# Performance work log

Hardware: AMD Instinct MI355X
Metric: run time of the kernel (lower is better)

Reference implementation:

```python
import jax, jax.numpy as jnp
import numpy as np
import math

B, L, D, H = 2, 2048, 1024, 16
HD = D // H

def setup_inputs() -> dict:
    key = jax.random.key(0)
    ks = jax.random.split(key, 8)
    s = 1.0 / math.sqrt(D)
    # causal additive mask: 0 on/below diagonal, -inf above
    causal = jnp.where(jnp.tril(jnp.ones((L, L), dtype=bool)), 0.0, -jnp.inf)
    causal = causal[None, None].astype(jnp.float32)  # [1,1,L,L]
    return {
        "Q": jax.random.normal(ks[0], (B, L, D), jnp.float32),
        "K": jax.random.normal(ks[1], (B, L, D), jnp.float32),
        "V": jax.random.normal(ks[2], (B, L, D), jnp.float32),
        "attn_mask": causal,
        "padding_mask": jnp.zeros((B, L), dtype=bool),
        "wq": jax.random.normal(ks[3], (D, D), jnp.float32) * s,
        "wk": jax.random.normal(ks[4], (D, D), jnp.float32) * s,
        "wv": jax.random.normal(ks[5], (D, D), jnp.float32) * s,
        "wout": jax.random.normal(ks[6], (D, D), jnp.float32) * s,
    }

def reference(Q, K, V, attn_mask, padding_mask, wq, wk, wv, wout):
    b, l, _ = Q.shape
    # projections (torch Linear: x @ W.T); weights sampled as [out,in]-like square
    def proj(x, w):
        return (x @ w.T).reshape(b, l, H, HD).transpose(0, 2, 1, 3)  # [B,H,L,hd]
    q = proj(Q, wq)
    k = proj(K, wk)
    v = proj(V, wv)
    scores = jnp.einsum("bhqd,bhkd->bhqk", q, k) / math.sqrt(HD)
    scores = scores + attn_mask
    scores = jnp.where(padding_mask[:, None, None, :], -jnp.inf, scores)
    weights = jax.nn.softmax(scores, axis=-1)
    ctx = jnp.einsum("bhqk,bhkd->bhqd", weights, v)
    ctx = ctx.transpose(0, 2, 1, 3).reshape(b, l, D)
    return ctx @ wout.T
```

## Files before the change

kernel.cpp:

```cpp
#include <hip/hip_runtime.h>
#include <stdint.h>
#include <stddef.h>

typedef __bf16 bf16_t;
typedef bf16_t bf16x4 __attribute__((ext_vector_type(4)));
typedef bf16_t bf16x8 __attribute__((ext_vector_type(8)));
typedef float f32x4 __attribute__((ext_vector_type(4)));

#define MFMA_BF16(A_, B_, C_) __builtin_amdgcn_mfma_f32_16x16x32_bf16(A_, B_, C_, 0, 0, 0)

static constexpr int Lseq = 2048;
static constexpr int Dmod = 1024;
static constexpr int Hn   = 16;
static constexpr int HDim = 64;
static constexpr size_t M1 = 1u << 20;

__device__ __forceinline__ int swz(int row, int chunk) {
  return row * 64 + ((chunk ^ (row & 7)) << 3);
}

__device__ __forceinline__ void async_ld16(const bf16_t* g, bf16_t* l) {
  __builtin_amdgcn_global_load_lds(
      (const __attribute__((address_space(1))) void*)g,
      (__attribute__((address_space(3))) void*)l, 16, 0, 0);
}

__global__ __launch_bounds__(256) void cvt_kernel(
    const float* __restrict__ Q, const float* __restrict__ K,
    const float* __restrict__ V, const float* __restrict__ wq,
    const float* __restrict__ wk, const float* __restrict__ wv,
    const float* __restrict__ wout, bf16_t* __restrict__ wsb)
{
  const int s = blockIdx.z;
  const float* __restrict__ src;
  if      (s < 4)   src = Q    + (size_t)s * M1;
  else if (s < 8)   src = K    + (size_t)(s - 4) * M1;
  else if (s < 12)  src = V    + (size_t)(s - 8) * M1;
  else if (s == 12) src = wq;
  else if (s == 13) src = wk;
  else if (s == 14) src = wv;
  else              src = wout;
  bf16_t* __restrict__ dst = wsb + (size_t)s * M1;

  const int t = blockIdx.x * 256 + threadIdx.x;
#pragma unroll
  for (int j = 0; j < 4; ++j) {
    const int i4 = t + j * 65536;
    float4 v4 = ((const float4*)src)[i4];
    bf16x4 b4;
    b4[0] = (bf16_t)v4.x; b4[1] = (bf16_t)v4.y;
    b4[2] = (bf16_t)v4.z; b4[3] = (bf16_t)v4.w;
    ((bf16x4*)dst)[i4] = b4;
  }
}

__global__ __launch_bounds__(256) void proj_kernel(
    const bf16_t* __restrict__ Qbf, const bf16_t* __restrict__ Kbf,
    const bf16_t* __restrict__ Vbf, const bf16_t* __restrict__ wqb,
    const bf16_t* __restrict__ wkb, const bf16_t* __restrict__ wvb,
    bf16_t* __restrict__ qo, bf16_t* __restrict__ ko, bf16_t* __restrict__ vo)
{
  const int z = blockIdx.z;
  const bf16_t* __restrict__ A  = (z == 0) ? Qbf : (z == 1) ? Kbf : Vbf;
  const bf16_t* __restrict__ Bw = (z == 0) ? wqb : (z == 1) ? wkb : wvb;
  bf16_t* __restrict__ dst      = (z == 0) ? qo  : (z == 1) ? ko  : vo;

  __shared__ __align__(16) bf16_t As[128 * 64];
  __shared__ __align__(16) bf16_t Bs[128 * 64];

  const int tid  = threadIdx.x;
  const int wave = tid >> 6;
  const int lane = tid & 63;
  const int quad = lane >> 4;
  const int l16  = lane & 15;
  const int wm   = (wave & 1) * 64;
  const int wn   = (wave >> 1) * 64;
  const int m0   = blockIdx.y * 128;
  const int n0   = blockIdx.x * 128;

  const int srow8  = lane >> 3;
  const int schunk = (lane & 7) ^ srow8;

  f32x4 acc[4][4];
#pragma unroll
  for (int i = 0; i < 4; ++i)
#pragma unroll
    for (int j = 0; j < 4; ++j)
#pragma unroll
      for (int e = 0; e < 4; ++e) acc[i][j][e] = 0.0f;

  for (int kt = 0; kt < 16; ++kt) {
    const int k0 = kt * 64;
    __syncthreads();
#pragma unroll
    for (int i = 0; i < 4; ++i) {
      const int rb = wave * 32 + i * 8;
      async_ld16(&A [(size_t)(m0 + rb + srow8) * Dmod + k0 + schunk * 8], &As[rb * 64]);
      async_ld16(&Bw[(size_t)(n0 + rb + srow8) * Dmod + k0 + schunk * 8], &Bs[rb * 64]);
    }
    __syncthreads();

    bf16x8 af[4][2], bfr[4][2];
#pragma unroll
    for (int mt = 0; mt < 4; ++mt) {
      const int row = wm + mt * 16 + l16;
      af[mt][0] = *(const bf16x8*)&As[swz(row, quad)];
      af[mt][1] = *(const bf16x8*)&As[swz(row, quad + 4)];
    }
#pragma unroll
    for (int nt = 0; nt < 4; ++nt) {
      const int row = wn + nt * 16 + l16;
      bfr[nt][0] = *(const bf16x8*)&Bs[swz(row, quad)];
      bfr[nt][1] = *(const bf16x8*)&Bs[swz(row, quad + 4)];
    }
#pragma unroll
    for (int mt = 0; mt < 4; ++mt)
#pragma unroll
      for (int nt = 0; nt < 4; ++nt) {
        acc[mt][nt] = MFMA_BF16(af[mt][0], bfr[nt][0], acc[mt][nt]);
        acc[mt][nt] = MFMA_BF16(af[mt][1], bfr[nt][1], acc[mt][nt]);
      }
  }

#pragma unroll
  for (int mt = 0; mt < 4; ++mt) {
    const int grb = m0 + wm + mt * 16 + quad * 4;
    const int bb  = grb >> 11;
    const int lb  = grb & 2047;
#pragma unroll
    for (int nt = 0; nt < 4; ++nt) {
      const int gc = n0 + wn + nt * 16 + l16;
      const int h  = gc >> 6;
      const int hd = gc & 63;
      if (z == 2) {
        bf16x4 pk;
#pragma unroll
        for (int r = 0; r < 4; ++r) pk[r] = (bf16_t)acc[mt][nt][r];
        *(bf16x4*)&dst[(((size_t)(bb * Hn + h) * HDim + hd) << 11) + lb] = pk;
      } else {
#pragma unroll
        for (int r = 0; r < 4; ++r)
          dst[(((size_t)(bb * Hn + h) * Lseq + lb + r) << 6) + hd] = (bf16_t)acc[mt][nt][r];
      }
    }
  }
}

__global__ __launch_bounds__(256) void attn_kernel(
    const bf16_t* __restrict__ q, const bf16_t* __restrict__ k,
    const bf16_t* __restrict__ v, bf16_t* __restrict__ ctx)
{
  const int px = blockIdx.x;
  const int bh = blockIdx.y;
  const int bb = bh >> 4;
  const int h  = bh & 15;

  const int tid  = threadIdx.x;
  const int wave = tid >> 6;
  const int lane = tid & 63;
  const int quad = lane >> 4;
  const int l16  = lane & 15;

  __shared__ __align__(16) bf16_t Ks[2][64 * 64];
  __shared__ __align__(16) bf16_t Vs[2][64 * 64];
  __shared__ __align__(16) bf16_t Ps[4][16][72];

  const bf16_t* __restrict__ qb = q + (size_t)bh * (Lseq * HDim);
  const bf16_t* __restrict__ kb = k + (size_t)bh * (Lseq * HDim);
  const bf16_t* __restrict__ vb = v + (size_t)bh * (HDim * Lseq);

  const int srow8  = lane >> 3;
  const int schunk = (lane & 7) ^ srow8;

  bf16x8 ones;
#pragma unroll
  for (int i = 0; i < 8; ++i) ones[i] = (bf16_t)1.0f;

  for (int half = 0; half < 2; ++half) {
    const int qt = half ? (31 - px) : px;
    const int q0 = qt * 64;
    const int qrow = q0 + wave * 16 + l16;

    bf16x8 qf0 = *(const bf16x8*)&qb[(size_t)qrow * HDim + quad * 8];
    bf16x8 qf1 = *(const bf16x8*)&qb[(size_t)qrow * HDim + 32 + quad * 8];

    f32x4 o[4];
    f32x4 lacc;
#pragma unroll
    for (int e = 0; e < 4; ++e) lacc[e] = 0.0f;
#pragma unroll
    for (int nt = 0; nt < 4; ++nt)
#pragma unroll
      for (int e = 0; e < 4; ++e) o[nt][e] = 0.0f;

    __syncthreads();
#pragma unroll
    for (int i = 0; i < 2; ++i) {
      const int rb = wave * 16 + i * 8;
      const int r  = rb + srow8;
      async_ld16(&kb[(size_t)r * HDim + schunk * 8], &Ks[0][rb * 64]);
      async_ld16(&vb[(size_t)r * Lseq + schunk * 8], &Vs[0][rb * 64]);
    }

    for (int jt = 0; jt <= qt; ++jt) {
      const int cur = jt & 1;
      __syncthreads();

      if (jt < qt) {
        const int j1 = (jt + 1) * 64;
#pragma unroll
        for (int i = 0; i < 2; ++i) {
          const int rb = wave * 16 + i * 8;
          const int r  = rb + srow8;
          async_ld16(&kb[(size_t)(j1 + r) * HDim + schunk * 8], &Ks[cur ^ 1][rb * 64]);
          async_ld16(&vb[(size_t)r * Lseq + j1 + schunk * 8], &Vs[cur ^ 1][rb * 64]);
        }
      }

      f32x4 s[4];
#pragma unroll
      for (int nt = 0; nt < 4; ++nt) {
#pragma unroll
        for (int e = 0; e < 4; ++e) s[nt][e] = 0.0f;
        const int krow = nt * 16 + l16;
        bf16x8 kf0 = *(const bf16x8*)&Ks[cur][swz(krow, quad)];
        bf16x8 kf1 = *(const bf16x8*)&Ks[cur][swz(krow, quad + 4)];
        s[nt] = MFMA_BF16(kf0, qf0, s[nt]);
        s[nt] = MFMA_BF16(kf1, qf1, s[nt]);
      }

      const bool diag = (jt == qt);
#pragma unroll
      for (int nt = 0; nt < 4; ++nt) {
        bf16x4 pk;
#pragma unroll
        for (int r = 0; r < 4; ++r) {
          float val = s[nt][r] * 0.18033688f;
          if (diag && (nt * 16 + quad * 4 + r > wave * 16 + l16)) val = -1e30f;
          pk[r] = (bf16_t)__builtin_amdgcn_exp2f(val);
        }
        *(bf16x4*)&Ps[wave][l16][nt * 16 + quad * 4] = pk;
      }

      bf16x8 pf0 = *(const bf16x8*)&Ps[wave][l16][quad * 8];
      bf16x8 pf1 = *(const bf16x8*)&Ps[wave][l16][32 + quad * 8];

      lacc = MFMA_BF16(pf0, ones, lacc);
      lacc = MFMA_BF16(pf1, ones, lacc);

#pragma unroll
      for (int nt = 0; nt < 4; ++nt) {
        const int vrow = nt * 16 + l16;
        bf16x8 vf0 = *(const bf16x8*)&Vs[cur][swz(vrow, quad)];
        bf16x8 vf1 = *(const bf16x8*)&Vs[cur][swz(vrow, quad + 4)];
        o[nt] = MFMA_BF16(pf0, vf0, o[nt]);
        o[nt] = MFMA_BF16(pf1, vf1, o[nt]);
      }
    }

    float inv[4];
#pragma unroll
    for (int r = 0; r < 4; ++r) inv[r] = 1.0f / lacc[r];
#pragma unroll
    for (int nt = 0; nt < 4; ++nt)
#pragma unroll
      for (int r = 0; r < 4; ++r) {
        const int gq = q0 + wave * 16 + quad * 4 + r;
        ctx[(size_t)(bb * Lseq + gq) * Dmod + h * HDim + nt * 16 + l16] =
            (bf16_t)(o[nt][r] * inv[r]);
      }
  }
}

__global__ __launch_bounds__(256) void out_kernel(
    const bf16_t* __restrict__ Actx, const bf16_t* __restrict__ Bwout,
    float* __restrict__ out)
{
  __shared__ __align__(16) bf16_t As[128 * 64];
  __shared__ __align__(16) bf16_t Bs[128 * 64];

  const int tid  = threadIdx.x;
  const int wave = tid >> 6;
  const int lane = tid & 63;
  const int quad = lane >> 4;
  const int l16  = lane & 15;
  const int wm   = (wave & 1) * 64;
  const int wn   = (wave >> 1) * 64;
  const int m0   = blockIdx.y * 128;
  const int n0   = blockIdx.x * 128;

  const int srow8  = lane >> 3;
  const int schunk = (lane & 7) ^ srow8;

  f32x4 acc[4][4];
#pragma unroll
  for (int i = 0; i < 4; ++i)
#pragma unroll
    for (int j = 0; j < 4; ++j)
#pragma unroll
      for (int e = 0; e < 4; ++e) acc[i][j][e] = 0.0f;

  for (int kt = 0; kt < 16; ++kt) {
    const int k0 = kt * 64;
    __syncthreads();
#pragma unroll
    for (int i = 0; i < 4; ++i) {
      const int rb = wave * 32 + i * 8;
      async_ld16(&Actx [(size_t)(m0 + rb + srow8) * Dmod + k0 + schunk * 8], &As[rb * 64]);
      async_ld16(&Bwout[(size_t)(n0 + rb + srow8) * Dmod + k0 + schunk * 8], &Bs[rb * 64]);
    }
    __syncthreads();

    bf16x8 af[4][2], bfr[4][2];
#pragma unroll
    for (int mt = 0; mt < 4; ++mt) {
      const int row = wm + mt * 16 + l16;
      af[mt][0] = *(const bf16x8*)&As[swz(row, quad)];
      af[mt][1] = *(const bf16x8*)&As[swz(row, quad + 4)];
    }
#pragma unroll
    for (int nt = 0; nt < 4; ++nt) {
      const int row = wn + nt * 16 + l16;
      bfr[nt][0] = *(const bf16x8*)&Bs[swz(row, quad)];
      bfr[nt][1] = *(const bf16x8*)&Bs[swz(row, quad + 4)];
    }
#pragma unroll
    for (int mt = 0; mt < 4; ++mt)
#pragma unroll
      for (int nt = 0; nt < 4; ++nt) {
        acc[mt][nt] = MFMA_BF16(af[mt][0], bfr[nt][0], acc[mt][nt]);
        acc[mt][nt] = MFMA_BF16(af[mt][1], bfr[nt][1], acc[mt][nt]);
      }
  }

#pragma unroll
  for (int mt = 0; mt < 4; ++mt) {
    const int grb = m0 + wm + mt * 16 + quad * 4;
#pragma unroll
    for (int nt = 0; nt < 4; ++nt) {
      const int gc = n0 + wn + nt * 16 + l16;
#pragma unroll
      for (int r = 0; r < 4; ++r)
        out[(size_t)(grb + r) * Dmod + gc] = acc[mt][nt][r];
    }
  }
}

extern "C" void kernel_launch(void* const* d_in, const int* in_sizes, int n_in,
                              void* d_out, int out_size, void* d_ws, size_t ws_size,
                              hipStream_t stream) {
  (void)in_sizes; (void)n_in; (void)out_size; (void)ws_size;
  const float* Q    = (const float*)d_in[0];
  const float* K    = (const float*)d_in[1];
  const float* V    = (const float*)d_in[2];
  const float* wq   = (const float*)d_in[5];
  const float* wk   = (const float*)d_in[6];
  const float* wv   = (const float*)d_in[7];
  const float* wout = (const float*)d_in[8];
  float* out = (float*)d_out;

  bf16_t* wsb = (bf16_t*)d_ws;
  bf16_t* Qbf   = wsb;
  bf16_t* Kbf   = wsb + 4 * M1;
  bf16_t* Vbf   = wsb + 8 * M1;
  bf16_t* wqb   = wsb + 12 * M1;
  bf16_t* wkb   = wsb + 13 * M1;
  bf16_t* wvb   = wsb + 14 * M1;
  bf16_t* woutb = wsb + 15 * M1;
  bf16_t* qp    = wsb + 16 * M1;
  bf16_t* kp    = wsb + 20 * M1;
  bf16_t* vp    = wsb + 24 * M1;
  bf16_t* cws   = wsb;

  cvt_kernel<<<dim3(256, 1, 16), 256, 0, stream>>>(Q, K, V, wq, wk, wv, wout, wsb);
  proj_kernel<<<dim3(8, 32, 3), 256, 0, stream>>>(Qbf, Kbf, Vbf, wqb, wkb, wvb, qp, kp, vp);
  attn_kernel<<<dim3(16, 32), 256, 0, stream>>>(qp, kp, vp, cws);
  out_kernel<<<dim3(8, 32), 256, 0, stream>>>(cws, woutb, out);
}
```

Measured before the change: 233.1 us.

## Double-buffer LDS tiles in projection and output GEMM kernels

Both the QKV projection kernel and the output projection kernel now keep two LDS buffers per operand. The next K-tile is prefetched with async global-to-LDS loads while MFMAs run on the current tile, and one barrier per iteration replaces two. The goal is to hide global load latency behind matrix math. In exchange, LDS per block doubles to 64 KB, which may lower occupancy. The compiler may also insert conservative vmcnt waits before LDS reads, which would remove the overlap.

```diff
diff --git a/kernel.cpp b/kernel.cpp
--- a/kernel.cpp
+++ b/kernel.cpp
@@ -65,8 +65,8 @@
   const bf16_t* __restrict__ Bw = (z == 0) ? wqb : (z == 1) ? wkb : wvb;
   bf16_t* __restrict__ dst      = (z == 0) ? qo  : (z == 1) ? ko  : vo;
 
-  __shared__ __align__(16) bf16_t As[128 * 64];
-  __shared__ __align__(16) bf16_t Bs[128 * 64];
+  __shared__ __align__(16) bf16_t As[2][128 * 64];
+  __shared__ __align__(16) bf16_t Bs[2][128 * 64];
 
   const int tid  = threadIdx.x;
   const int wave = tid >> 6;
@@ -89,29 +89,39 @@
 #pragma unroll
       for (int e = 0; e < 4; ++e) acc[i][j][e] = 0.0f;
 
+#pragma unroll
+  for (int i = 0; i < 4; ++i) {
+    const int rb = wave * 32 + i * 8;
+    async_ld16(&A [(size_t)(m0 + rb + srow8) * Dmod + schunk * 8], &As[0][rb * 64]);
+    async_ld16(&Bw[(size_t)(n0 + rb + srow8) * Dmod + schunk * 8], &Bs[0][rb * 64]);
+  }
+
   for (int kt = 0; kt < 16; ++kt) {
-    const int k0 = kt * 64;
+    const int cur = kt & 1;
     __syncthreads();
-#pragma unroll
-    for (int i = 0; i < 4; ++i) {
-      const int rb = wave * 32 + i * 8;
-      async_ld16(&A [(size_t)(m0 + rb + srow8) * Dmod + k0 + schunk * 8], &As[rb * 64]);
-      async_ld16(&Bw[(size_t)(n0 + rb + srow8) * Dmod + k0 + schunk * 8], &Bs[rb * 64]);
-    }
-    __syncthreads();
+
+    if (kt < 15) {
+      const int k1 = (kt + 1) * 64;
+#pragma unroll
+      for (int i = 0; i < 4; ++i) {
+        const int rb = wave * 32 + i * 8;
+        async_ld16(&A [(size_t)(m0 + rb + srow8) * Dmod + k1 + schunk * 8], &As[cur ^ 1][rb * 64]);
+        async_ld16(&Bw[(size_t)(n0 + rb + srow8) * Dmod + k1 + schunk * 8], &Bs[cur ^ 1][rb * 64]);
+      }
+    }
 
     bf16x8 af[4][2], bfr[4][2];
 #pragma unroll
     for (int mt = 0; mt < 4; ++mt) {
       const int row = wm + mt * 16 + l16;
-      af[mt][0] = *(const bf16x8*)&As[swz(row, quad)];
-      af[mt][1] = *(const bf16x8*)&As[swz(row, quad + 4)];
+      af[mt][0] = *(const bf16x8*)&As[cur][swz(row, quad)];
+      af[mt][1] = *(const bf16x8*)&As[cur][swz(row, quad + 4)];
     }
 #pragma unroll
     for (int nt = 0; nt < 4; ++nt) {
       const int row = wn + nt * 16 + l16;
-      bfr[nt][0] = *(const bf16x8*)&Bs[swz(row, quad)];
-      bfr[nt][1] = *(const bf16x8*)&Bs[swz(row, quad + 4)];
+      bfr[nt][0] = *(const bf16x8*)&Bs[cur][swz(row, quad)];
+      bfr[nt][1] = *(const bf16x8*)&Bs[cur][swz(row, quad + 4)];
     }
 #pragma unroll
     for (int mt = 0; mt < 4; ++mt)
@@ -276,8 +286,8 @@
     const bf16_t* __restrict__ Actx, const bf16_t* __restrict__ Bwout,
     float* __restrict__ out)
 {
-  __shared__ __align__(16) bf16_t As[128 * 64];
-  __shared__ __align__(16) bf16_t Bs[128 * 64];
+  __shared__ __align__(16) bf16_t As[2][128 * 64];
+  __shared__ __align__(16) bf16_t Bs[2][128 * 64];
 
   const int tid  = threadIdx.x;
   const int wave = tid >> 6;
@@ -300,29 +310,39 @@
 #pragma unroll
       for (int e = 0; e < 4; ++e) acc[i][j][e] = 0.0f;
 
+#pragma unroll
+  for (int i = 0; i < 4; ++i) {
+    const int rb = wave * 32 + i * 8;
+    async_ld16(&Actx [(size_t)(m0 + rb + srow8) * Dmod + schunk * 8], &As[0][rb * 64]);
+    async_ld16(&Bwout[(size_t)(n0 + rb + srow8) * Dmod + schunk * 8], &Bs[0][rb * 64]);
+  }
+
   for (int kt = 0; kt < 16; ++kt) {
-    const int k0 = kt * 64;
+    const int cur = kt & 1;
     __syncthreads();
-#pragma unroll
-    for (int i = 0; i < 4; ++i) {
-      const int rb = wave * 32 + i * 8;
-      async_ld16(&Actx [(size_t)(m0 + rb + srow8) * Dmod + k0 + schunk * 8], &As[rb * 64]);
-      async_ld16(&Bwout[(size_t)(n0 + rb + srow8) * Dmod + k0 + schunk * 8], &Bs[rb * 64]);
-    }
-    __syncthreads();
+
+    if (kt < 15) {
+      const int k1 = (kt + 1) * 64;
+#pragma unroll
+      for (int i = 0; i < 4; ++i) {
+        const int rb = wave * 32 + i * 8;
+        async_ld16(&Actx [(size_t)(m0 + rb + srow8) * Dmod + k1 + schunk * 8], &As[cur ^ 1][rb * 64]);
+        async_ld16(&Bwout[(size_t)(n0 + rb + srow8) * Dmod + k1 + schunk * 8], &Bs[cur ^ 1][rb * 64]);
+      }
+    }
 
     bf16x8 af[4][2], bfr[4][2];
 #pragma unroll
     for (int mt = 0; mt < 4; ++mt) {
       const int row = wm + mt * 16 + l16;
-      af[mt][0] = *(const bf16x8*)&As[swz(row, quad)];
-      af[mt][1] = *(const bf16x8*)&As[swz(row, quad + 4)];
+      af[mt][0] = *(const bf16x8*)&As[cur][swz(row, quad)];
+      af[mt][1] = *(const bf16x8*)&As[cur][swz(row, quad + 4)];
     }
 #pragma unroll
     for (int nt = 0; nt < 4; ++nt) {
       const int row = wn + nt * 16 + l16;
-      bfr[nt][0] = *(const bf16x8*)&Bs[swz(row, quad)];
-      bfr[nt][1] = *(const bf16x8*)&Bs[swz(row, quad + 4)];
+      bfr[nt][0] = *(const bf16x8*)&Bs[cur][swz(row, quad)];
+      bfr[nt][1] = *(const bf16x8*)&Bs[cur][swz(row, quad + 4)];
     }
 #pragma unroll
     for (int mt = 0; mt < 4; ++mt)
```

New measurement: 235.8 us. No clear change (+1.2%).
